# Kernel tuning notes

Hardware: AMD Instinct MI355X
Metric: run time of the kernel (lower is better)

Reference implementation:

```python
import jax, jax.numpy as jnp
from jax import lax
import numpy as np

B, C, Hf, Wf = 4, 256, 64, 64
COMP = max(C // 4, 16)  # 64
SCALE, K_UP, K_ENC = 2, 5, 3
EPS = 1e-5


def setup_inputs() -> dict:
    key = jax.random.key(0)
    ks = jax.random.split(key, 6)
    x = jax.random.normal(ks[0], (B, C, Hf, Wf), dtype=jnp.float32)
    w_comp = jax.random.normal(ks[1], (COMP, C), dtype=jnp.float32) * (1.0 / np.sqrt(C))
    bn_gamma = jnp.ones((COMP,), dtype=jnp.float32)
    bn_beta = jnp.zeros((COMP,), dtype=jnp.float32)
    bn_mean = jax.random.normal(ks[2], (COMP,), dtype=jnp.float32) * 0.1
    bn_var = jax.random.uniform(ks[3], (COMP,), dtype=jnp.float32, minval=0.5, maxval=1.5)
    w_enc = jax.random.normal(ks[4], (K_UP * K_UP * SCALE * SCALE, COMP, K_ENC, K_ENC), dtype=jnp.float32) * (1.0 / np.sqrt(COMP * K_ENC * K_ENC))
    return {"x": x, "w_comp": w_comp, "bn_gamma": bn_gamma, "bn_beta": bn_beta,
            "bn_mean": bn_mean, "bn_var": bn_var, "w_enc": w_enc}


def reference(x, w_comp, bn_gamma, bn_beta, bn_mean, bn_var, w_enc):
    b, c, h, w = x.shape
    s, k = SCALE, K_UP
    # 1x1 compression conv
    comp = jnp.einsum('bchw,oc->bohw', x, w_comp)
    # BatchNorm (eval-style, running stats) + SiLU
    inv = (bn_gamma / jnp.sqrt(bn_var + EPS))[:, None, None]
    bn = (comp - bn_mean[:, None, None]) * inv + bn_beta[:, None, None]
    act = bn * jax.nn.sigmoid(bn)
    # encoder conv -> per-pixel reassembly kernels, channels = k^2 * s^2 (k2 outer, s2 inner)
    mask = lax.conv_general_dilated(act, w_enc, (1, 1), ((1, 1), (1, 1)),
                                    dimension_numbers=('NCHW', 'OIHW', 'NCHW'))
    mask = mask.reshape(b, k * k, s * s, h, w)
    mask = jax.nn.softmax(mask, axis=1)  # softmax over k_up*k_up window
    # unfold: gather 5x5 neighborhoods (pad 2), k = dy*5+dx row-major like F.unfold
    pad = k // 2
    xp = jnp.pad(x, ((0, 0), (0, 0), (pad, pad), (pad, pad)))
    patches = jnp.stack([xp[:, :, dy:dy + h, dx:dx + w]
                         for dy in range(k) for dx in range(k)], axis=2)  # (b,c,k2,h,w)
    # content-aware weighted sum per sub-pixel position
    out = jnp.einsum('bksij,bckij->bcsij', mask, patches)  # (b,c,s2,h,w)
    # s2 -> (s0,s1); pixel (i*s+s0, j*s+s1)
    out = out.reshape(b, c, s, s, h, w).transpose(0, 1, 4, 2, 5, 3).reshape(b, c, h * s, w * s)
    return out
```

## Files before the change

### kernel.cpp

```cpp
#include <hip/hip_runtime.h>
#include <hip/hip_bf16.h>
#include <math.h>

#define B_ 4
#define C_ 256
#define H_ 64
#define W_ 64
#define COMP_ 64
#define K2_ 25
#define HW_ (H_*W_)
#define EPS_ 1e-5f
#define WTE_STRIDE 26

typedef float v2f __attribute__((ext_vector_type(2)));
#define FMA2(a, b, c) __builtin_elementwise_fma((a), (b), (c))

__global__ void k_transpose(const float* __restrict__ w_comp,
                            const float* __restrict__ w_enc,
                            float* __restrict__ wTc,
                            float* __restrict__ wTe) {
    int t = blockIdx.x * 256 + threadIdx.x;
    if (t < COMP_ * C_) {
        int o = t & 63;
        int c = t >> 6;
        wTc[t] = w_comp[o * C_ + c];
    } else {
        int t2 = t - COMP_ * C_;
        if (t2 < 100 * COMP_ * 9) {
            int k2 = t2 % 25;
            int r = t2 / 25;
            int s2 = r & 3; r >>= 2;
            int q = r % 9;
            int o = r / 9;
            wTe[((o * 9 + q) * 4 + s2) * WTE_STRIDE + k2] =
                w_enc[(((k2 * 4 + s2) * COMP_) + o) * 9 + q];
        }
    }
}

__global__ void __launch_bounds__(1024)
k_compress(const float* __restrict__ x, const float* __restrict__ wTc,
           const float* __restrict__ gamma, const float* __restrict__ beta,
           const float* __restrict__ mean, const float* __restrict__ var,
           float* __restrict__ act) {
    __shared__ v2f redA[32 * 64];
    __shared__ v2f redB[32 * 64];
    const int tx = threadIdx.x;
    const int ty = threadIdx.y;
    const int tz = threadIdx.z;
    const int ogu = __builtin_amdgcn_readfirstlane(ty);
    const int cgu = __builtin_amdgcn_readfirstlane(tz);
    const int b = blockIdx.y;
    const int p0 = blockIdx.x * 64;

    v2f acc2[8];
#pragma unroll
    for (int k = 0; k < 8; ++k) acc2[k] = (v2f){0.f, 0.f};

    const float* xb = x + (size_t)b * C_ * HW_ + p0 + tx;
#pragma unroll 4
    for (int cl = 0; cl < 64; ++cl) {
        int c = cgu * 64 + cl;
        float xv = xb[c * HW_];
        const v2f* w2 = (const v2f*)(wTc + c * COMP_ + ogu * 16);
        v2f xv2 = (v2f){xv, xv};
#pragma unroll
        for (int k = 0; k < 8; ++k)
            acc2[k] = FMA2(xv2, w2[k], acc2[k]);
    }

    const int rbase = ty * 8;
    if (tz == 1) {
#pragma unroll
        for (int k = 0; k < 8; ++k) redA[(rbase + k) * 64 + tx] = acc2[k];
    } else if (tz == 2) {
#pragma unroll
        for (int k = 0; k < 8; ++k) redB[(rbase + k) * 64 + tx] = acc2[k];
    }
    __syncthreads();
    if (tz == 0) {
#pragma unroll
        for (int k = 0; k < 8; ++k) acc2[k] += redA[(rbase + k) * 64 + tx];
    } else if (tz == 3) {
#pragma unroll
        for (int k = 0; k < 8; ++k) acc2[k] += redB[(rbase + k) * 64 + tx];
    }
    __syncthreads();
    if (tz == 3) {
#pragma unroll
        for (int k = 0; k < 8; ++k) redA[(rbase + k) * 64 + tx] = acc2[k];
    }
    __syncthreads();
    if (tz == 0) {
#pragma unroll
        for (int k = 0; k < 8; ++k) {
            v2f s = acc2[k] + redA[(rbase + k) * 64 + tx];
            int o0 = ty * 16 + 2 * k;
#pragma unroll
            for (int h = 0; h < 2; ++h) {
                int o = o0 + h;
                float sv = (h == 0) ? s.x : s.y;
                float iv = gamma[o] * rsqrtf(var[o] + EPS_);
                float bn = (sv - mean[o]) * iv + beta[o];
                float sg = 1.f / (1.f + __expf(-bn));
                act[((b * COMP_ + o) * HW_) + p0 + tx] = bn * sg;
            }
        }
    }
}

__global__ void __launch_bounds__(1024)
k_encoder(const float* __restrict__ act, const float* __restrict__ wTe,
          float* __restrict__ maskT) {
    __shared__ float sact[13312];
    const int tx = threadIdx.x;
    const int ty = threadIdx.y;
    const int tz = threadIdx.z;
    const int tid = (tz * 4 + ty) * 64 + tx;
    const int i = blockIdx.x;
    const int b = blockIdx.y;
    const int s2u = __builtin_amdgcn_readfirstlane(ty);
    const int ogu = __builtin_amdgcn_readfirstlane(tz);

    const float* ab = act + (size_t)b * COMP_ * HW_;
    for (int t = tid; t < 3 * COMP_ * 66; t += 1024) {
        int col = t % 66;
        int r = t / 66;
        int o = r & 63;
        int row = r >> 6;
        int gi = i + row - 1;
        int gj = col - 1;
        float v = 0.f;
        if ((unsigned)gi < 64u && (unsigned)gj < 64u)
            v = ab[(o * H_ + gi) * W_ + gj];
        sact[t] = v;
    }
    __syncthreads();

    v2f acc2[13];
#pragma unroll
    for (int k = 0; k < 13; ++k) acc2[k] = (v2f){0.f, 0.f};

#pragma unroll 1
    for (int oi = 0; oi < 16; ++oi) {
        int o = ogu * 16 + oi;
#pragma unroll
        for (int q = 0; q < 9; ++q) {
            const int dy = q / 3, dx = q % 3;
            float a = sact[(dy * COMP_ + o) * 66 + tx + dx];
            const float* wb = wTe + ((o * 9 + q) * 4 + s2u) * WTE_STRIDE;
            const v2f* w2 = (const v2f*)wb;
            v2f a2 = (v2f){a, a};
#pragma unroll
            for (int k = 0; k < 12; ++k)
                acc2[k] = FMA2(a2, w2[k], acc2[k]);
            acc2[12].x = fmaf(wb[24], a, acc2[12].x);
        }
    }
    __syncthreads();

    v2f* bufA = (v2f*)sact;
    v2f* bufB = bufA + 3328;
    const int rix = ty * 64 + tx;
    if (tz == 1) {
#pragma unroll
        for (int k = 0; k < 13; ++k) bufA[k * 256 + rix] = acc2[k];
    } else if (tz == 2) {
#pragma unroll
        for (int k = 0; k < 13; ++k) bufB[k * 256 + rix] = acc2[k];
    }
    __syncthreads();
    if (tz == 0) {
#pragma unroll
        for (int k = 0; k < 13; ++k) acc2[k] += bufA[k * 256 + rix];
    } else if (tz == 3) {
#pragma unroll
        for (int k = 0; k < 13; ++k) acc2[k] += bufB[k * 256 + rix];
    }
    __syncthreads();
    if (tz == 3) {
#pragma unroll
        for (int k = 0; k < 13; ++k) bufA[k * 256 + rix] = acc2[k];
    }
    __syncthreads();
    float ex[K2_];
    if (tz == 0) {
#pragma unroll
        for (int k = 0; k < 13; ++k) acc2[k] += bufA[k * 256 + rix];

        float mx = acc2[12].x;
#pragma unroll
        for (int k = 0; k < 12; ++k) mx = fmaxf(mx, fmaxf(acc2[k].x, acc2[k].y));
        float sum = 0.f;
#pragma unroll
        for (int k = 0; k < 12; ++k) {
            ex[2 * k]     = __expf(acc2[k].x - mx);
            ex[2 * k + 1] = __expf(acc2[k].y - mx);
            sum += ex[2 * k] + ex[2 * k + 1];
        }
        ex[24] = __expf(acc2[12].x - mx);
        sum += ex[24];
        float rs = 1.f / sum;
#pragma unroll
        for (int k = 0; k < K2_; ++k) ex[k] *= rs;
    }
    __syncthreads();

    float* st = sact;
    if (tz == 0) {
#pragma unroll
        for (int k = 0; k < K2_; ++k)
            st[tx * 100 + k * 4 + ty] = ex[k];
    }
    __syncthreads();

    float4* dst = (float4*)(maskT + ((size_t)b * HW_ + i * 64) * 100);
    const float4* src = (const float4*)st;
    for (int t = tid; t < 1600; t += 1024)
        dst[t] = src[t];
}

__global__ void __launch_bounds__(256)
k_reassemble(const float* __restrict__ x, const float* __restrict__ maskT,
             float* __restrict__ out) {
    __shared__ __align__(16) float smask[64 * 100];
    __shared__ __align__(16) float sx[5 * 68 * 20];
    const int tx = threadIdx.x;
    const int ty = threadIdx.y;
    const int tid = ty * 64 + tx;
    const int i = blockIdx.x;
    const int cc = blockIdx.y;
    const int b = blockIdx.z;

    {
        const float4* src = (const float4*)(maskT + ((size_t)b * HW_ + i * 64) * 100);
        float4* dst = (float4*)smask;
#pragma unroll
        for (int t = 0; t < 7; ++t) {
            int e = tid + t * 256;
            if (e < 1600) dst[e] = src[e];
        }
    }

    const float* xb = x + ((size_t)b * C_ + cc * 16 + ty * 4) * HW_;
#pragma unroll
    for (int r = 0; r < 5; ++r) {
        const int gi = i + r - 2;
        const bool rowok = ((unsigned)gi < 64u);
        {
            float4 v = {0.f, 0.f, 0.f, 0.f};
            int gj = tx - 2;
            if (rowok && gj >= 0) {
                const float* p = xb + gi * W_ + gj;
                v.x = p[0];
                v.y = p[HW_];
                v.z = p[2 * HW_];
                v.w = p[3 * HW_];
            }
            *(float4*)&sx[(r * 68 + tx) * 20 + ty * 4] = v;
        }
        if (tid < 16) {
            int q = tid >> 2;
            int col = 64 + (tid & 3);
            int gj = col - 2;
            float4 v = {0.f, 0.f, 0.f, 0.f};
            if (rowok && gj < 64) {
                const float* p = x + ((size_t)b * C_ + cc * 16 + q * 4) * HW_ + gi * W_ + gj;
                v.x = p[0];
                v.y = p[HW_];
                v.z = p[2 * HW_];
                v.w = p[3 * HW_];
            }
            *(float4*)&sx[(r * 68 + col) * 20 + q * 4] = v;
        }
    }
    __syncthreads();

    v2f a01[4], a23[4];
#pragma unroll
    for (int cl = 0; cl < 4; ++cl) { a01[cl] = (v2f){0.f, 0.f}; a23[cl] = (v2f){0.f, 0.f}; }

    float4 xq = *(const float4*)&sx[(0 * 68 + tx + 0) * 20 + ty * 4];
    float4 m  = *(const float4*)&smask[tx * 100 + 0];

#pragma unroll
    for (int k2 = 0; k2 < K2_; ++k2) {
        float4 xq_c = xq, m_c = m;
        if (k2 < K2_ - 1) {
            const int kn = k2 + 1;
            const int dy = kn / 5, dx = kn % 5;
            xq = *(const float4*)&sx[(dy * 68 + tx + dx) * 20 + ty * 4];
            m  = *(const float4*)&smask[tx * 100 + kn * 4];
        }
        v2f m01 = (v2f){m_c.x, m_c.y};
        v2f m23 = (v2f){m_c.z, m_c.w};
        float xc[4] = {xq_c.x, xq_c.y, xq_c.z, xq_c.w};
#pragma unroll
        for (int cl = 0; cl < 4; ++cl) {
            v2f xv2 = (v2f){xc[cl], xc[cl]};
            a01[cl] = FMA2(xv2, m01, a01[cl]);
            a23[cl] = FMA2(xv2, m23, a23[cl]);
        }
    }

#pragma unroll
    for (int cl = 0; cl < 4; ++cl) {
        int c = cc * 16 + ty * 4 + cl;
        float* op = out + (((size_t)(b * C_ + c) * 128 + 2 * i) * 128) + 2 * tx;
        *(float2*)op         = float2{a01[cl].x, a01[cl].y};
        *(float2*)(op + 128) = float2{a23[cl].x, a23[cl].y};
    }
}

extern "C" void kernel_launch(void* const* d_in, const int* in_sizes, int n_in,
                              void* d_out, int out_size, void* d_ws, size_t ws_size,
                              hipStream_t stream) {
    const float* x       = (const float*)d_in[0];
    const float* w_comp  = (const float*)d_in[1];
    const float* bn_g    = (const float*)d_in[2];
    const float* bn_b    = (const float*)d_in[3];
    const float* bn_m    = (const float*)d_in[4];
    const float* bn_v    = (const float*)d_in[5];
    const float* w_enc   = (const float*)d_in[6];
    float* out = (float*)d_out;

    float* ws    = (float*)d_ws;
    float* wTc   = ws;
    float* wTe   = ws + 16384;
    float* act   = ws + 16384 + 59904;
    float* maskT = act + (size_t)B_ * COMP_ * HW_;

    k_transpose<<<289, 256, 0, stream>>>(w_comp, w_enc, wTc, wTe);
    k_compress<<<dim3(64, B_), dim3(64, 4, 4), 0, stream>>>(x, wTc, bn_g, bn_b, bn_m, bn_v, act);
    k_encoder<<<dim3(64, B_), dim3(64, 4, 4), 0, stream>>>(act, wTe, maskT);
    k_reassemble<<<dim3(64, 16, B_), dim3(64, 4), 0, stream>>>(x, maskT, out);
}
```

Measured before the change: 171.7 us.

## Store softmax mask in fp16 and rebalance compress reduction split

The softmax mask written by the encoder and read by the reassembly kernel is now stored as fp16, which halves that intermediate's global traffic and its shared-memory footprint. The compress kernel's thread layout changes from 4 output groups by 4 channel groups to 8 by 2, so only one shared-memory reduction step is needed instead of three barrier-separated stages. The encoder's outer channel loop is also unrolled by 2. Mask values lose precision to fp16 rounding, which may add small errors to the output.

New measurement: 168.9 us. No clear change (-1.6%).

```diff
diff --git a/kernel.cpp b/kernel.cpp
--- a/kernel.cpp
+++ b/kernel.cpp
@@ -1,5 +1,6 @@
 #include <hip/hip_runtime.h>
 #include <hip/hip_bf16.h>
+#include <hip/hip_fp16.h>
 #include <math.h>
 
 #define B_ 4
@@ -43,8 +44,7 @@
            const float* __restrict__ gamma, const float* __restrict__ beta,
            const float* __restrict__ mean, const float* __restrict__ var,
            float* __restrict__ act) {
-    __shared__ v2f redA[32 * 64];
-    __shared__ v2f redB[32 * 64];
+    __shared__ v2f red[32 * 64];
     const int tx = threadIdx.x;
     const int ty = threadIdx.y;
     const int tz = threadIdx.z;
@@ -53,49 +53,32 @@
     const int b = blockIdx.y;
     const int p0 = blockIdx.x * 64;
 
-    v2f acc2[8];
-#pragma unroll
-    for (int k = 0; k < 8; ++k) acc2[k] = (v2f){0.f, 0.f};
+    v2f acc2[4];
+#pragma unroll
+    for (int k = 0; k < 4; ++k) acc2[k] = (v2f){0.f, 0.f};
 
     const float* xb = x + (size_t)b * C_ * HW_ + p0 + tx;
-#pragma unroll 4
-    for (int cl = 0; cl < 64; ++cl) {
-        int c = cgu * 64 + cl;
+#pragma unroll 8
+    for (int cl = 0; cl < 128; ++cl) {
+        int c = cgu * 128 + cl;
         float xv = xb[c * HW_];
-        const v2f* w2 = (const v2f*)(wTc + c * COMP_ + ogu * 16);
+        const v2f* w2 = (const v2f*)(wTc + c * COMP_ + ogu * 8);
         v2f xv2 = (v2f){xv, xv};
 #pragma unroll
-        for (int k = 0; k < 8; ++k)
+        for (int k = 0; k < 4; ++k)
             acc2[k] = FMA2(xv2, w2[k], acc2[k]);
     }
 
-    const int rbase = ty * 8;
     if (tz == 1) {
 #pragma unroll
-        for (int k = 0; k < 8; ++k) redA[(rbase + k) * 64 + tx] = acc2[k];
-    } else if (tz == 2) {
-#pragma unroll
-        for (int k = 0; k < 8; ++k) redB[(rbase + k) * 64 + tx] = acc2[k];
+        for (int k = 0; k < 4; ++k) red[(ty * 4 + k) * 64 + tx] = acc2[k];
     }
     __syncthreads();
     if (tz == 0) {
 #pragma unroll
-        for (int k = 0; k < 8; ++k) acc2[k] += redA[(rbase + k) * 64 + tx];
-    } else if (tz == 3) {
-#pragma unroll
-        for (int k = 0; k < 8; ++k) acc2[k] += redB[(rbase + k) * 64 + tx];
-    }
-    __syncthreads();
-    if (tz == 3) {
-#pragma unroll
-        for (int k = 0; k < 8; ++k) redA[(rbase + k) * 64 + tx] = acc2[k];
-    }
-    __syncthreads();
-    if (tz == 0) {
-#pragma unroll
-        for (int k = 0; k < 8; ++k) {
-            v2f s = acc2[k] + redA[(rbase + k) * 64 + tx];
-            int o0 = ty * 16 + 2 * k;
+        for (int k = 0; k < 4; ++k) {
+            v2f s = acc2[k] + red[(ty * 4 + k) * 64 + tx];
+            int o0 = ty * 8 + 2 * k;
 #pragma unroll
             for (int h = 0; h < 2; ++h) {
                 int o = o0 + h;
@@ -111,7 +94,7 @@
 
 __global__ void __launch_bounds__(1024)
 k_encoder(const float* __restrict__ act, const float* __restrict__ wTe,
-          float* __restrict__ maskT) {
+          __half* __restrict__ maskT) {
     __shared__ float sact[13312];
     const int tx = threadIdx.x;
     const int ty = threadIdx.y;
@@ -141,7 +124,7 @@
 #pragma unroll
     for (int k = 0; k < 13; ++k) acc2[k] = (v2f){0.f, 0.f};
 
-#pragma unroll 1
+#pragma unroll 2
     for (int oi = 0; oi < 16; ++oi) {
         int o = ogu * 16 + oi;
 #pragma unroll
@@ -206,24 +189,23 @@
     }
     __syncthreads();
 
-    float* st = sact;
+    __half* st = (__half*)sact;
     if (tz == 0) {
 #pragma unroll
         for (int k = 0; k < K2_; ++k)
-            st[tx * 100 + k * 4 + ty] = ex[k];
+            st[tx * 100 + k * 4 + ty] = __float2half(ex[k]);
     }
     __syncthreads();
 
     float4* dst = (float4*)(maskT + ((size_t)b * HW_ + i * 64) * 100);
     const float4* src = (const float4*)st;
-    for (int t = tid; t < 1600; t += 1024)
-        dst[t] = src[t];
+    if (tid < 800) dst[tid] = src[tid];
 }
 
 __global__ void __launch_bounds__(256)
-k_reassemble(const float* __restrict__ x, const float* __restrict__ maskT,
+k_reassemble(const float* __restrict__ x, const __half* __restrict__ maskT,
              float* __restrict__ out) {
-    __shared__ __align__(16) float smask[64 * 100];
+    __shared__ __align__(16) __half smask[64 * 100];
     __shared__ __align__(16) float sx[5 * 68 * 20];
     const int tx = threadIdx.x;
     const int ty = threadIdx.y;
@@ -236,9 +218,9 @@
         const float4* src = (const float4*)(maskT + ((size_t)b * HW_ + i * 64) * 100);
         float4* dst = (float4*)smask;
 #pragma unroll
-        for (int t = 0; t < 7; ++t) {
+        for (int t = 0; t < 4; ++t) {
             int e = tid + t * 256;
-            if (e < 1600) dst[e] = src[e];
+            if (e < 800) dst[e] = src[e];
         }
     }
 
@@ -281,19 +263,24 @@
     for (int cl = 0; cl < 4; ++cl) { a01[cl] = (v2f){0.f, 0.f}; a23[cl] = (v2f){0.f, 0.f}; }
 
     float4 xq = *(const float4*)&sx[(0 * 68 + tx + 0) * 20 + ty * 4];
-    float4 m  = *(const float4*)&smask[tx * 100 + 0];
+    __half2 h01 = *(const __half2*)&smask[tx * 100 + 0];
+    __half2 h23 = *(const __half2*)&smask[tx * 100 + 2];
 
 #pragma unroll
     for (int k2 = 0; k2 < K2_; ++k2) {
-        float4 xq_c = xq, m_c = m;
+        float4 xq_c = xq;
+        __half2 h01_c = h01, h23_c = h23;
         if (k2 < K2_ - 1) {
             const int kn = k2 + 1;
             const int dy = kn / 5, dx = kn % 5;
-            xq = *(const float4*)&sx[(dy * 68 + tx + dx) * 20 + ty * 4];
-            m  = *(const float4*)&smask[tx * 100 + kn * 4];
-        }
-        v2f m01 = (v2f){m_c.x, m_c.y};
-        v2f m23 = (v2f){m_c.z, m_c.w};
+            xq  = *(const float4*)&sx[(dy * 68 + tx + dx) * 20 + ty * 4];
+            h01 = *(const __half2*)&smask[tx * 100 + kn * 4];
+            h23 = *(const __half2*)&smask[tx * 100 + kn * 4 + 2];
+        }
+        float2 f01 = __half22float2(h01_c);
+        float2 f23 = __half22float2(h23_c);
+        v2f m01 = (v2f){f01.x, f01.y};
+        v2f m23 = (v2f){f23.x, f23.y};
         float xc[4] = {xq_c.x, xq_c.y, xq_c.z, xq_c.w};
 #pragma unroll
         for (int cl = 0; cl < 4; ++cl) {
@@ -328,10 +315,10 @@
     float* wTc   = ws;
     float* wTe   = ws + 16384;
     float* act   = ws + 16384 + 59904;
-    float* maskT = act + (size_t)B_ * COMP_ * HW_;
+    __half* maskT = (__half*)(act + (size_t)B_ * COMP_ * HW_);
 
     k_transpose<<<289, 256, 0, stream>>>(w_comp, w_enc, wTc, wTe);
-    k_compress<<<dim3(64, B_), dim3(64, 4, 4), 0, stream>>>(x, wTc, bn_g, bn_b, bn_m, bn_v, act);
+    k_compress<<<dim3(64, B_), dim3(64, 8, 2), 0, stream>>>(x, wTc, bn_g, bn_b, bn_m, bn_v, act);
     k_encoder<<<dim3(64, B_), dim3(64, 4, 4), 0, stream>>>(act, wTe, maskT);
     k_reassemble<<<dim3(64, 16, B_), dim3(64, 4), 0, stream>>>(x, maskT, out);
 }
```
